# Kernel optimization log

Measured on AMD Instinct MI355X. Metric: run time of the kernel, lower is better.

## Reference

```python
import jax, jax.numpy as jnp
import numpy as np
import math

B, C, H, W = 16, 512, 32, 32
HEADS = 8
HD = C // HEADS            # 64 head_dim
NFREQ = HD // 4            # 16 (head_dim % 4 == 0)
MAX_FREQ = 128.0
T = H * W                  # 1024 tokens


def _make_so2_mat():
    # make_2dcoord: meshgrid('ij') of arange(H), arange(W) -> [H, W, 2]
    xg, yg = np.meshgrid(np.arange(H, dtype=np.float32), np.arange(W, dtype=np.float32), indexing='ij')
    coord = np.stack([xg, yg], -1)                                   # [H, W, 2]
    freqs = np.exp(np.linspace(0.0, math.log(MAX_FREQ), NFREQ)).astype(np.float32)  # [NFREQ]
    th = coord[..., None, :] * freqs[None, None, :, None]            # [H, W, NFREQ, 2]
    c, s = np.cos(th), np.sin(th)
    # rotation matrices [[c, -s], [s, c]] -> [H, W, NFREQ, 2(dim), 2, 2]
    mat = np.stack([np.stack([c, -s], -1), np.stack([s, c], -1)], -2)
    mat = mat.reshape(H * W, NFREQ * 2, 2, 2)                        # flatten(2,3) then flatten(0,1)
    return jnp.asarray(mat[:, : HD // 2])                            # [T, HD//2, 2, 2]


def setup_inputs() -> dict:
    key = jax.random.key(0)
    ks = jax.random.split(key, 5)
    mat = _make_so2_mat()
    return {
        'x': jax.random.normal(ks[0], (B, C, H, W), dtype=jnp.float32),
        'w_qkv': jax.random.normal(ks[1], (3 * C, C), dtype=jnp.float32) * 0.02,
        'b_qkv': jax.random.normal(ks[2], (3 * C,), dtype=jnp.float32) * 0.02,
        'w_o': jax.random.normal(ks[3], (C, C), dtype=jnp.float32) * 0.02,
        'b_o': jax.random.normal(ks[4], (C,), dtype=jnp.float32) * 0.02,
        'mat_q': mat,
        'mat_k': mat,
        'mat_v': mat,
        'mat_o': jnp.swapaxes(mat, -2, -1),
    }


def _rep_mul(rep, t):
    # rep: [T, HD//2, 2, 2]; t: [B, nh, T, HD] -> per-pair 2x2 rotation
    tb = t.reshape(B, HEADS, T, HD // 2, 2)
    return jnp.einsum('tfij,bntfj->bntfi', rep, tb).reshape(B, HEADS, T, HD)


def _split_heads(t):
    # 'b (c nh) h w -> b nh (h w) c' (c outer, nh inner in channel dim)
    return t.reshape(B, HD, HEADS, T).transpose(0, 2, 3, 1)


def reference(x, w_qkv, b_qkv, w_o, b_o, mat_q, mat_k, mat_v, mat_o):
    # 1x1 conv QKV projection == channel GEMM
    qkv = jnp.einsum('bchw,oc->bohw', x, w_qkv) + b_qkv[None, :, None, None]
    q, k, v = jnp.split(qkv, 3, axis=1)
    q, k, v = map(_split_heads, (q, k, v))                 # [B, nh, T, HD]
    q = _rep_mul(mat_q, q)
    k = _rep_mul(mat_k, k)
    v = _rep_mul(mat_v, v)
    scale = 1.0 / math.sqrt(HD)
    attn = jax.nn.softmax(jnp.einsum('bntd,bnsd->bnts', q, k) * scale, axis=-1)
    o = jnp.einsum('bnts,bnsd->bntd', attn, v)             # [B, nh, T, HD]
    o = _rep_mul(mat_o, o)
    # 'b nh (h w) c -> b (c nh) h w'
    o = o.reshape(B, HEADS, H, W, HD).transpose(0, 4, 1, 2, 3).reshape(B, C, H, W)
    return jnp.einsum('bchw,oc->bohw', o, w_o) + b_o[None, :, None, None]
```

## Files before the change

kernel.cpp:

```cpp
#include <hip/hip_runtime.h>


typedef __bf16 bf16x8 __attribute__((ext_vector_type(8)));
typedef float  f32x4  __attribute__((ext_vector_type(4)));

__device__ __forceinline__ f32x4 mfma16(bf16x8 a, bf16x8 b, f32x4 c) {
    return __builtin_amdgcn_mfma_f32_16x16x32_bf16(a, b, c, 0, 0, 0);
}

__device__ __forceinline__ void async16(const void* g, void* l) {
    __builtin_amdgcn_global_load_lds(
        (const __attribute__((address_space(1))) void*)g,
        (__attribute__((address_space(3))) void*)l, 16, 0, 0);
}

__global__ void k_convert_w(const float* __restrict__ wq, const float* __restrict__ wo,
                            __bf16* __restrict__ wqb, __bf16* __restrict__ wob) {
    int i = blockIdx.x * 256 + threadIdx.x;
    if (i < 3 * 512 * 512) wqb[i] = (__bf16)wq[i];
    if (i < 512 * 512)     wob[i] = (__bf16)wo[i];
}

__global__ void k_transpose_x(const float* __restrict__ x, __bf16* __restrict__ xt) {
    __shared__ float tile[32][33];
    const int b  = blockIdx.z;
    const int c0 = blockIdx.y * 32;
    const int t0 = blockIdx.x * 32;
    const int tx = threadIdx.x, ty = threadIdx.y;
    const float* xp = x + ((size_t)b * 512 + c0) * 1024 + t0;
#pragma unroll
    for (int j = 0; j < 4; j++)
        tile[ty + j * 8][tx] = xp[(ty + j * 8) * 1024 + tx];
    __syncthreads();
    __bf16* xo = xt + ((size_t)b * 1024 + t0) * 512 + c0;
#pragma unroll
    for (int j = 0; j < 4; j++)
        xo[(ty + j * 8) * 512 + tx] = (__bf16)tile[tx][ty + j * 8];
}

__global__ __launch_bounds__(256) void k_gemm_qkv(
        const __bf16* __restrict__ A, const __bf16* __restrict__ W,
        const float* __restrict__ bias,
        const float* __restrict__ matq, const float* __restrict__ matk,
        const float* __restrict__ matv,
        __bf16* __restrict__ qd, __bf16* __restrict__ kd, __bf16* __restrict__ vtd)
{
    __shared__ __bf16 As[128][64];
    __shared__ __bf16 Bs[128][64];
    const int tid = threadIdx.x;
    const int m0 = blockIdx.x * 128;
    const int jb = blockIdx.y;
    const int part = jb >> 2;
    const int nh_base = (jb & 3) * 2;
    const int lane = tid & 63, w = tid >> 6;
    const int ln = lane & 15, quad = lane >> 4;
    const int wr = w >> 1, wc = w & 1;

    const int srow = lane >> 3;
    const int scol = (((lane & 7) ^ srow) * 8);

    const __bf16* arow[4];
    const __bf16* brow[4];
#pragma unroll
    for (int jj = 0; jj < 4; jj++) {
        int rr = w * 32 + jj * 8 + srow;
        arow[jj] = &A[(size_t)(m0 + rr) * 512 + scol];
        int o = part * 512 + (rr & 63) * 8 + nh_base + (rr >> 6);
        brow[jj] = &W[(size_t)o * 512 + scol];
    }

    f32x4 acc[4][4] = {};

    for (int k0 = 0; k0 < 512; k0 += 64) {
#pragma unroll
        for (int jj = 0; jj < 4; jj++)
            async16(arow[jj] + k0, &As[w * 32 + jj * 8][0]);
#pragma unroll
        for (int jj = 0; jj < 4; jj++)
            async16(brow[jj] + k0, &Bs[w * 32 + jj * 8][0]);
        __syncthreads();
#pragma unroll
        for (int h = 0; h < 2; h++) {
            bf16x8 af[4], wf[4];
#pragma unroll
            for (int mi = 0; mi < 4; mi++)
                af[mi] = *(const bf16x8*)&As[wr * 64 + mi * 16 + ln][(((h * 4 + quad) ^ (ln & 7)) * 8)];
#pragma unroll
            for (int ni = 0; ni < 4; ni++)
                wf[ni] = *(const bf16x8*)&Bs[wc * 64 + ni * 16 + ln][(((h * 4 + quad) ^ (ln & 7)) * 8)];
#pragma unroll
            for (int mi = 0; mi < 4; mi++)
#pragma unroll
                for (int ni = 0; ni < 4; ni++)
                    acc[mi][ni] = mfma16(af[mi], wf[ni], acc[mi][ni]);
        }
        __syncthreads();
    }

    const int nh = nh_base + wc;
    const int rowbase = m0 + wr * 64;
    const int b  = rowbase >> 10, t0 = rowbase & 1023;
    const int bh = b * 8 + nh;
    const int ip = ln & 1;
    const float2* matp = (const float2*)(part == 0 ? matq : (part == 1 ? matk : matv));
    __bf16* qkdst = (part == 0) ? qd : kd;

#pragma unroll
    for (int ni = 0; ni < 4; ni++) {
        const int hd = ni * 16 + ln;
        const int f  = hd >> 1;
        const float bias_o = bias[part * 512 + hd * 8 + nh];
#pragma unroll
        for (int mi = 0; mi < 4; mi++) {
            const int tq = t0 + mi * 16 + quad * 4;
            if (part < 2) {
#pragma unroll
                for (int r = 0; r < 4; r++) {
                    int t = tq + r;
                    float val = acc[mi][ni][r] + bias_o;
                    float pr  = __shfl_xor(val, 1);
                    float2 mv = matp[((size_t)t * 32 + f) * 2 + ip];
                    float e  = ip ? pr : val;
                    float oo = ip ? val : pr;
                    float rv = mv.x * e + mv.y * oo;
                    qkdst[((size_t)bh * 1024 + t) * 64 + hd] = (__bf16)rv;
                }
            } else {
                __bf16 pack[4];
#pragma unroll
                for (int r = 0; r < 4; r++) {
                    int t = tq + r;
                    float val = acc[mi][ni][r] + bias_o;
                    float pr  = __shfl_xor(val, 1);
                    float2 mv = matp[((size_t)t * 32 + f) * 2 + ip];
                    float e  = ip ? pr : val;
                    float oo = ip ? val : pr;
                    pack[r] = (__bf16)(mv.x * e + mv.y * oo);
                }
                *(uint2*)&vtd[((size_t)bh * 64 + hd) * 1024 + tq] = *(const uint2*)pack;
            }
        }
    }
}

__global__ __launch_bounds__(256) void k_attn(
        const __bf16* __restrict__ q, const __bf16* __restrict__ kk,
        const __bf16* __restrict__ vt, const float* __restrict__ mato,
        __bf16* __restrict__ od)
{
    __shared__ __bf16 Ks[64][72];
    __shared__ __bf16 Vs[64][72];
    __shared__ __bf16 Ps[4][32][72];
    const int qt = blockIdx.x, nh = blockIdx.y, b = blockIdx.z;
    const int bh = b * 8 + nh;
    const int tid = threadIdx.x, w = tid >> 6, lane = tid & 63;
    const int ln = lane & 15, quad = lane >> 4;
    const int qr0 = qt * 128 + w * 32;

    bf16x8 qa[2][2];
#pragma unroll
    for (int mi = 0; mi < 2; mi++)
#pragma unroll
        for (int ki = 0; ki < 2; ki++)
            qa[mi][ki] = *(const bf16x8*)&q[((size_t)bh * 1024 + qr0 + mi * 16 + ln) * 64 + ki * 32 + quad * 8];

    f32x4 oacc[2][4] = {};
    float lr[2][4] = {};

    const float C_EXP = 0.18033688011112042f;

    for (int st = 0; st < 16; st++) {
#pragma unroll
        for (int c = 0; c < 2; c++) {
            int idx = tid + c * 256;
            int row = idx >> 3, g = (idx & 7) * 8;
            *(bf16x8*)&Ks[row][g] = *(const bf16x8*)&kk[((size_t)bh * 1024 + st * 64 + row) * 64 + g];
            *(bf16x8*)&Vs[row][g] = *(const bf16x8*)&vt[((size_t)bh * 64 + row) * 1024 + st * 64 + g];
        }
        __syncthreads();

        f32x4 s[2][4] = {};
#pragma unroll
        for (int si = 0; si < 4; si++) {
            bf16x8 kb0 = *(const bf16x8*)&Ks[si * 16 + ln][quad * 8];
            bf16x8 kb1 = *(const bf16x8*)&Ks[si * 16 + ln][32 + quad * 8];
#pragma unroll
            for (int mi = 0; mi < 2; mi++) {
                s[mi][si] = mfma16(qa[mi][0], kb0, s[mi][si]);
                s[mi][si] = mfma16(qa[mi][1], kb1, s[mi][si]);
            }
        }

#pragma unroll
        for (int mi = 0; mi < 2; mi++)
#pragma unroll
            for (int si = 0; si < 4; si++)
#pragma unroll
                for (int r = 0; r < 4; r++) {
                    float p = exp2f(s[mi][si][r] * C_EXP);
                    lr[mi][r] += p;
                    Ps[w][mi * 16 + quad * 4 + r][si * 16 + ln] = (__bf16)p;
                }

#pragma unroll
        for (int kt = 0; kt < 2; kt++) {
            bf16x8 pa0 = *(const bf16x8*)&Ps[w][ln][kt * 32 + quad * 8];
            bf16x8 pa1 = *(const bf16x8*)&Ps[w][16 + ln][kt * 32 + quad * 8];
#pragma unroll
            for (int ni = 0; ni < 4; ni++) {
                bf16x8 vb = *(const bf16x8*)&Vs[ni * 16 + ln][kt * 32 + quad * 8];
                oacc[0][ni] = mfma16(pa0, vb, oacc[0][ni]);
                oacc[1][ni] = mfma16(pa1, vb, oacc[1][ni]);
            }
        }
        __syncthreads();
    }

    float inv[2][4];
#pragma unroll
    for (int mi = 0; mi < 2; mi++)
#pragma unroll
        for (int r = 0; r < 4; r++) {
            float v = lr[mi][r];
#pragma unroll
            for (int d = 1; d <= 8; d <<= 1) v += __shfl_xor(v, d);
            inv[mi][r] = 1.0f / v;
        }

    const float2* mo2 = (const float2*)mato;
#pragma unroll
    for (int mi = 0; mi < 2; mi++) {
#pragma unroll
        for (int ni = 0; ni < 4; ni++) {
            int hd = ni * 16 + ln;
            int f = hd >> 1, ip = ln & 1;
#pragma unroll
            for (int r = 0; r < 4; r++) {
                int t = qr0 + mi * 16 + quad * 4 + r;
                float val = oacc[mi][ni][r] * inv[mi][r];
                float pr  = __shfl_xor(val, 1);
                float2 mv = mo2[(t * 32 + f) * 2 + ip];
                float e  = ip ? pr : val;
                float oo = ip ? val : pr;
                float rv = mv.x * e + mv.y * oo;
                od[((size_t)b * 1024 + t) * 512 + hd * 8 + nh] = (__bf16)rv;
            }
        }
    }
}

__global__ __launch_bounds__(256) void k_gemm_out(
        const __bf16* __restrict__ A, const __bf16* __restrict__ W,
        const float* __restrict__ bias, float* __restrict__ out)
{
    __shared__ __bf16 As[128][64];
    __shared__ __bf16 Bs[128][64];
    const int tid = threadIdx.x;
    const int m0 = blockIdx.x * 128;
    const int n0 = blockIdx.y * 128;
    const int lane = tid & 63, w = tid >> 6;
    const int ln = lane & 15, quad = lane >> 4;
    const int wr = w >> 1, wc = w & 1;

    const int srow = lane >> 3;
    const int scol = (((lane & 7) ^ srow) * 8);

    const __bf16* arow[4];
    const __bf16* brow[4];
#pragma unroll
    for (int jj = 0; jj < 4; jj++) {
        int rr = w * 32 + jj * 8 + srow;
        arow[jj] = &A[(size_t)(m0 + rr) * 512 + scol];
        brow[jj] = &W[(size_t)(n0 + rr) * 512 + scol];
    }

    f32x4 acc[4][4] = {};

    for (int k0 = 0; k0 < 512; k0 += 64) {
#pragma unroll
        for (int jj = 0; jj < 4; jj++)
            async16(arow[jj] + k0, &As[w * 32 + jj * 8][0]);
#pragma unroll
        for (int jj = 0; jj < 4; jj++)
            async16(brow[jj] + k0, &Bs[w * 32 + jj * 8][0]);
        __syncthreads();
#pragma unroll
        for (int h = 0; h < 2; h++) {
            bf16x8 af[4], wf[4];
#pragma unroll
            for (int mi = 0; mi < 4; mi++)
                af[mi] = *(const bf16x8*)&As[wr * 64 + mi * 16 + ln][(((h * 4 + quad) ^ (ln & 7)) * 8)];
#pragma unroll
            for (int ni = 0; ni < 4; ni++)
                wf[ni] = *(const bf16x8*)&Bs[wc * 64 + ni * 16 + ln][(((h * 4 + quad) ^ (ln & 7)) * 8)];
#pragma unroll
            for (int mi = 0; mi < 4; mi++)
#pragma unroll
                for (int ni = 0; ni < 4; ni++)
                    acc[mi][ni] = mfma16(af[mi], wf[ni], acc[mi][ni]);
        }
        __syncthreads();
    }

    const int rowbase = m0 + wr * 64;
    const int bb = rowbase >> 10, t0 = rowbase & 1023;
#pragma unroll
    for (int ni = 0; ni < 4; ni++) {
        int o = n0 + wc * 64 + ni * 16 + ln;
        float bias_o = bias[o];
#pragma unroll
        for (int mi = 0; mi < 4; mi++) {
            int t = t0 + mi * 16 + quad * 4;
            f32x4 v = acc[mi][ni];
            v[0] += bias_o; v[1] += bias_o; v[2] += bias_o; v[3] += bias_o;
            *(f32x4*)&out[((size_t)bb * 512 + o) * 1024 + t] = v;
        }
    }
}

extern "C" void kernel_launch(void* const* d_in, const int* in_sizes, int n_in,
                              void* d_out, int out_size, void* d_ws, size_t ws_size,
                              hipStream_t stream) {
    (void)in_sizes; (void)n_in; (void)out_size; (void)ws_size;
    const float* x     = (const float*)d_in[0];
    const float* w_qkv = (const float*)d_in[1];
    const float* b_qkv = (const float*)d_in[2];
    const float* w_o   = (const float*)d_in[3];
    const float* b_o   = (const float*)d_in[4];
    const float* mat_q = (const float*)d_in[5];
    const float* mat_k = (const float*)d_in[6];
    const float* mat_v = (const float*)d_in[7];
    const float* mat_o = (const float*)d_in[8];
    float* out = (float*)d_out;

    char* p = (char*)d_ws;
    __bf16* wqb = (__bf16*)p;  p += (size_t)3 * 512 * 512 * 2;
    __bf16* wob = (__bf16*)p;  p += (size_t)512 * 512 * 2;
    char* xt_base = p;
    __bf16* xt  = (__bf16*)p;  p += (size_t)16384 * 512 * 2;
    __bf16* qd  = (__bf16*)p;  p += (size_t)128 * 1024 * 64 * 2;
    __bf16* kd  = (__bf16*)p;  p += (size_t)128 * 1024 * 64 * 2;
    __bf16* vtd = (__bf16*)p;  p += (size_t)128 * 64 * 1024 * 2;
    __bf16* od  = (__bf16*)xt_base;

    k_convert_w  <<<dim3(3072),       dim3(256),    0, stream>>>(w_qkv, w_o, wqb, wob);
    k_transpose_x<<<dim3(32, 16, 16), dim3(32, 8),  0, stream>>>(x, xt);
    k_gemm_qkv   <<<dim3(128, 12),    dim3(256),    0, stream>>>(xt, wqb, b_qkv, mat_q, mat_k, mat_v, qd, kd, vtd);
    k_attn       <<<dim3(8, 8, 16),   dim3(256),    0, stream>>>(qd, kd, vtd, mat_o, od);
    k_gemm_out   <<<dim3(128, 4),     dim3(256),    0, stream>>>(od, wob, b_o, out);
}
```

Before: 243.7 us.

## Rework attention tile loading with async LDS loads, XOR swizzle, MFMA row sums

Rewrites the attention inner loop so K and V tiles are loaded straight into shared memory with async global-to-LDS loads, and uses an XOR-swizzled unpadded layout in place of padded rows. The score MFMA now has its operands swapped so each lane writes P as packed 4-wide stores. Softmax row sums are computed by an extra MFMA against a ones vector, which removes the per-element adds and the shuffle reduction. The grid is reordered so the batch-head index is fastest, which changes how blocks that share K/V are placed. The risks are extra MFMA work and correctness depending on the swizzle and the async-load lane mapping.

```diff
diff --git a/kernel.cpp b/kernel.cpp
--- a/kernel.cpp
+++ b/kernel.cpp
@@ -2,6 +2,7 @@
 
 
 typedef __bf16 bf16x8 __attribute__((ext_vector_type(8)));
+typedef __bf16 bf16x4 __attribute__((ext_vector_type(4)));
 typedef float  f32x4  __attribute__((ext_vector_type(4)));
 
 __device__ __forceinline__ f32x4 mfma16(bf16x8 a, bf16x8 b, f32x4 c) {
@@ -148,13 +149,16 @@
         const __bf16* __restrict__ vt, const float* __restrict__ mato,
         __bf16* __restrict__ od)
 {
-    __shared__ __bf16 Ks[64][72];
-    __shared__ __bf16 Vs[64][72];
-    __shared__ __bf16 Ps[4][32][72];
-    const int qt = blockIdx.x, nh = blockIdx.y, b = blockIdx.z;
-    const int bh = b * 8 + nh;
+    __shared__ __bf16 Ks[64][64];
+    __shared__ __bf16 Vs[64][64];
+    __shared__ __bf16 Ps[4][32][64];
+    const int bh = blockIdx.x, qt = blockIdx.y;
+    const int b = bh >> 3;
     const int tid = threadIdx.x, w = tid >> 6, lane = tid & 63;
     const int ln = lane & 15, quad = lane >> 4;
+    const int lx = ln & 7;
+    const int srow = lane >> 3;
+    const int scol = ((lane & 7) ^ srow) * 8;
     const int qr0 = qt * 128 + w * 32;
 
     bf16x8 qa[2][2];
@@ -164,54 +168,61 @@
         for (int ki = 0; ki < 2; ki++)
             qa[mi][ki] = *(const bf16x8*)&q[((size_t)bh * 1024 + qr0 + mi * 16 + ln) * 64 + ki * 32 + quad * 8];
 
+    const __bf16* kbase = kk + (size_t)bh * 1024 * 64;
+    const __bf16* vbase = vt + (size_t)bh * 64 * 1024;
+
     f32x4 oacc[2][4] = {};
-    float lr[2][4] = {};
-
+    f32x4 lacc[2] = {};
     const float C_EXP = 0.18033688011112042f;
 
+    bf16x8 ones;
+#pragma unroll
+    for (int j = 0; j < 8; j++) ones[j] = (__bf16)1.0f;
+
     for (int st = 0; st < 16; st++) {
 #pragma unroll
-        for (int c = 0; c < 2; c++) {
-            int idx = tid + c * 256;
-            int row = idx >> 3, g = (idx & 7) * 8;
-            *(bf16x8*)&Ks[row][g] = *(const bf16x8*)&kk[((size_t)bh * 1024 + st * 64 + row) * 64 + g];
-            *(bf16x8*)&Vs[row][g] = *(const bf16x8*)&vt[((size_t)bh * 64 + row) * 1024 + st * 64 + g];
-        }
-        __syncthreads();
-
-        f32x4 s[2][4] = {};
+        for (int i = 0; i < 2; i++) {
+            int r0 = w * 16 + i * 8;
+            async16(kbase + (size_t)(st * 64 + r0 + srow) * 64 + scol, &Ks[r0][0]);
+            async16(vbase + (size_t)(r0 + srow) * 1024 + st * 64 + scol, &Vs[r0][0]);
+        }
+        __syncthreads();
+
 #pragma unroll
         for (int si = 0; si < 4; si++) {
-            bf16x8 kb0 = *(const bf16x8*)&Ks[si * 16 + ln][quad * 8];
-            bf16x8 kb1 = *(const bf16x8*)&Ks[si * 16 + ln][32 + quad * 8];
+            bf16x8 kb0 = *(const bf16x8*)&Ks[si * 16 + ln][((quad    ) ^ lx) * 8];
+            bf16x8 kb1 = *(const bf16x8*)&Ks[si * 16 + ln][((quad + 4) ^ lx) * 8];
+            f32x4 sc[2] = {};
 #pragma unroll
             for (int mi = 0; mi < 2; mi++) {
-                s[mi][si] = mfma16(qa[mi][0], kb0, s[mi][si]);
-                s[mi][si] = mfma16(qa[mi][1], kb1, s[mi][si]);
-            }
-        }
-
-#pragma unroll
-        for (int mi = 0; mi < 2; mi++)
-#pragma unroll
-            for (int si = 0; si < 4; si++)
-#pragma unroll
-                for (int r = 0; r < 4; r++) {
-                    float p = exp2f(s[mi][si][r] * C_EXP);
-                    lr[mi][r] += p;
-                    Ps[w][mi * 16 + quad * 4 + r][si * 16 + ln] = (__bf16)p;
-                }
+                sc[mi] = mfma16(kb0, qa[mi][0], sc[mi]);
+                sc[mi] = mfma16(kb1, qa[mi][1], sc[mi]);
+            }
+#pragma unroll
+            for (int mi = 0; mi < 2; mi++) {
+                bf16x4 pk;
+#pragma unroll
+                for (int r = 0; r < 4; r++)
+                    pk[r] = (__bf16)exp2f(sc[mi][r] * C_EXP);
+                *(bf16x4*)((char*)&Ps[w][mi * 16 + ln][0]
+                           + (((si * 2 + (quad >> 1)) ^ lx) * 16) + (quad & 1) * 8) = pk;
+            }
+        }
 
 #pragma unroll
         for (int kt = 0; kt < 2; kt++) {
-            bf16x8 pa0 = *(const bf16x8*)&Ps[w][ln][kt * 32 + quad * 8];
-            bf16x8 pa1 = *(const bf16x8*)&Ps[w][16 + ln][kt * 32 + quad * 8];
+            bf16x8 pa[2];
+#pragma unroll
+            for (int mi = 0; mi < 2; mi++)
+                pa[mi] = *(const bf16x8*)&Ps[w][mi * 16 + ln][((kt * 4 + quad) ^ lx) * 8];
 #pragma unroll
             for (int ni = 0; ni < 4; ni++) {
-                bf16x8 vb = *(const bf16x8*)&Vs[ni * 16 + ln][kt * 32 + quad * 8];
-                oacc[0][ni] = mfma16(pa0, vb, oacc[0][ni]);
-                oacc[1][ni] = mfma16(pa1, vb, oacc[1][ni]);
-            }
+                bf16x8 vb = *(const bf16x8*)&Vs[ni * 16 + ln][((kt * 4 + quad) ^ lx) * 8];
+                oacc[0][ni] = mfma16(pa[0], vb, oacc[0][ni]);
+                oacc[1][ni] = mfma16(pa[1], vb, oacc[1][ni]);
+            }
+            lacc[0] = mfma16(pa[0], ones, lacc[0]);
+            lacc[1] = mfma16(pa[1], ones, lacc[1]);
         }
         __syncthreads();
     }
@@ -220,13 +231,10 @@
 #pragma unroll
     for (int mi = 0; mi < 2; mi++)
 #pragma unroll
-        for (int r = 0; r < 4; r++) {
-            float v = lr[mi][r];
-#pragma unroll
-            for (int d = 1; d <= 8; d <<= 1) v += __shfl_xor(v, d);
-            inv[mi][r] = 1.0f / v;
-        }
-
+        for (int r = 0; r < 4; r++)
+            inv[mi][r] = 1.0f / lacc[mi][r];
+
+    const int nh = bh & 7;
     const float2* mo2 = (const float2*)mato;
 #pragma unroll
     for (int mi = 0; mi < 2; mi++) {
@@ -346,6 +354,6 @@
     k_convert_w  <<<dim3(3072),       dim3(256),    0, stream>>>(w_qkv, w_o, wqb, wob);
     k_transpose_x<<<dim3(32, 16, 16), dim3(32, 8),  0, stream>>>(x, xt);
     k_gemm_qkv   <<<dim3(128, 12),    dim3(256),    0, stream>>>(xt, wqb, b_qkv, mat_q, mat_k, mat_v, qd, kd, vtd);
-    k_attn       <<<dim3(8, 8, 16),   dim3(256),    0, stream>>>(qd, kd, vtd, mat_o, od);
+    k_attn       <<<dim3(128, 8),     dim3(256),    0, stream>>>(qd, kd, vtd, mat_o, od);
     k_gemm_out   <<<dim3(128, 4),     dim3(256),    0, stream>>>(od, wob, b_o, out);
 }
```

Measured after the change: 250.1 us. +2.6%, slower.
